# Performance work log

Measured on AMD Instinct MI355X. Metric: run time of the kernel, lower is better.

## Reference

```python
import jax, jax.numpy as jnp
import numpy as np

N_NODES = 100000
N_EDGES = 1600000
IN_RAW = 64
HID = 128


def setup_inputs() -> dict:
    key = jax.random.key(0)
    ks = jax.random.split(key, 16)
    inp = {
        "x": jax.random.normal(ks[0], (N_NODES, IN_RAW), dtype=jnp.float32),
        "edge_index": jax.random.randint(ks[1], (2, N_EDGES), 0, N_NODES, dtype=jnp.int64),
        "user_ids": jax.random.randint(ks[2], (N_NODES,), 0, 10000, dtype=jnp.int64),
        "locations": jax.random.randint(ks[3], (N_NODES,), 0, 1000, dtype=jnp.int64),
        "time_features": jax.random.normal(ks[4], (N_NODES, 4), dtype=jnp.float32),
        # embeddings / encoders
        "user_emb_table": jax.random.normal(ks[5], (10000, 32), dtype=jnp.float32) * 0.02,
        "loc_emb_table": jax.random.normal(ks[6], (1000, 16), dtype=jnp.float32) * 0.02,
        "W_time": jax.random.normal(ks[7], (4, 16), dtype=jnp.float32) * 0.1,
        "b_time": jnp.zeros((16,), dtype=jnp.float32),
        # SAGEConv 1: lin_l (aggregated, with bias), lin_r (root, no bias)
        "W1_l": jax.random.normal(ks[8], (HID, HID), dtype=jnp.float32) * (1.0 / np.sqrt(HID)),
        "b1": jnp.zeros((HID,), dtype=jnp.float32),
        "W1_r": jax.random.normal(ks[9], (HID, HID), dtype=jnp.float32) * (1.0 / np.sqrt(HID)),
        # SAGEConv 2
        "W2_l": jax.random.normal(ks[10], (HID, HID), dtype=jnp.float32) * (1.0 / np.sqrt(HID)),
        "b2": jnp.zeros((HID,), dtype=jnp.float32),
        "W2_r": jax.random.normal(ks[11], (HID, HID), dtype=jnp.float32) * (1.0 / np.sqrt(HID)),
        # classifier
        "Wc": jax.random.normal(ks[12], (HID, 1), dtype=jnp.float32) * (1.0 / np.sqrt(HID)),
        "bc": jnp.zeros((1,), dtype=jnp.float32),
    }
    return inp


def _sage_conv(h, src, dst, W_l, b_l, W_r, n_nodes):
    # mean aggregation of source features onto targets (PyG SAGEConv default)
    msg_sum = jax.ops.segment_sum(h[src], dst, num_segments=n_nodes)  # [N, D]
    deg = jax.ops.segment_sum(jnp.ones((src.shape[0],), h.dtype), dst, num_segments=n_nodes)
    agg = msg_sum / jnp.maximum(deg, 1.0)[:, None]
    return agg @ W_l + b_l + h @ W_r


def reference(x, edge_index, user_ids, locations, time_features,
              user_emb_table, loc_emb_table, W_time, b_time,
              W1_l, b1, W1_r, W2_l, b2, W2_r, Wc, bc):
    n = x.shape[0]
    src, dst = edge_index[0], edge_index[1]
    user_emb = user_emb_table[user_ids]            # [N, 32]
    loc_emb = loc_emb_table[locations]             # [N, 16]
    time_emb = time_features @ W_time + b_time     # [N, 16]
    h = jnp.concatenate([x, user_emb, loc_emb, time_emb], axis=-1)  # [N, 128]
    h = jax.nn.relu(_sage_conv(h, src, dst, W1_l, b1, W1_r, n))  # dropout = identity (eval)
    h = jax.nn.relu(_sage_conv(h, src, dst, W2_l, b2, W2_r, n))
    return jax.nn.sigmoid(h @ Wc + bc)  # [N, 1]
```

## Files before the change

kernel.cpp:

```cpp
#include <hip/hip_runtime.h>
#include <math.h>

#define N_NODES 100000
#define HID 128
#define NB 782
#define CAP 4096
#define NBLK 256
#define BTILE 6250
#define SUBCAP 32
#define SCAP 3072
#define WPB 64
#define EBLK 3125

typedef __attribute__((ext_vector_type(8))) short bf16x8;
typedef __attribute__((ext_vector_type(4))) float f32x4;
typedef __attribute__((ext_vector_type(2))) float f32x2;

__device__ __forceinline__ unsigned short f2bf(float f) {
  union { float f; unsigned u; } v; v.f = f;
  unsigned r = v.u + 0x7FFFu + ((v.u >> 16) & 1u);
  return (unsigned short)(r >> 16);
}
__device__ __forceinline__ unsigned packbf(float lo, float hi) {
  return (unsigned)f2bf(lo) | ((unsigned)f2bf(hi) << 16);
}
__device__ __forceinline__ unsigned pkfp8x4(float a, float b, float c, float d) {
  int v = __builtin_amdgcn_cvt_pk_fp8_f32(a, b, 0, false);
  v = __builtin_amdgcn_cvt_pk_fp8_f32(c, d, v, true);
  return (unsigned)v;
}
__device__ __forceinline__ float bflo(unsigned u) {
  union { unsigned u; float f; } v; v.u = u << 16; return v.f;
}
__device__ __forceinline__ float bfhi(unsigned u) {
  union { unsigned u; float f; } v; v.u = u & 0xFFFF0000u; return v.f;
}
__device__ __forceinline__ void acc_add_fp8(float* a, unsigned w) {
  f32x2 p0 = __builtin_amdgcn_cvt_pk_f32_fp8((int)w, false);
  f32x2 p1 = __builtin_amdgcn_cvt_pk_f32_fp8((int)w, true);
  a[0] += p0.x; a[1] += p0.y; a[2] += p1.x; a[3] += p1.y;
}
__device__ __forceinline__ void acc_add_row(float* a, uint4 u) {
  acc_add_fp8(a + 0, u.x);
  acc_add_fp8(a + 4, u.y);
  acc_add_fp8(a + 8, u.z);
  acc_add_fp8(a + 12, u.w);
}

__global__ __launch_bounds__(512) void k_bktembed(
    const int* __restrict__ src, const int* __restrict__ dst,
    int* __restrict__ gcnt, unsigned* __restrict__ bdata2, int E,
    const float* __restrict__ x, const int* __restrict__ uid,
    const int* __restrict__ lid, const float* __restrict__ timef,
    const float* __restrict__ utab, const float* __restrict__ ltab,
    const float* __restrict__ Wt, const float* __restrict__ bt,
    unsigned short* __restrict__ h0, unsigned char* __restrict__ h0f8) {
  __shared__ int hcnt[NB];
  int t = threadIdx.x;
  if (blockIdx.x < NBLK) {
    int blk = blockIdx.x;
    int e0 = blk * BTILE;
    int e1 = min(e0 + BTILE, E);
    for (int i = t; i < NB; i += 512) hcnt[i] = 0;
    __syncthreads();
#pragma unroll 4
    for (int e = e0 + t; e < e1; e += 512) {
      int d = dst[e], s = src[e];
      int b = d >> 7;
      int pos = atomicAdd(&hcnt[b], 1);
      if (pos < SUBCAP)
        bdata2[((size_t)blk * NB + b) * SUBCAP + pos] =
            ((unsigned)s << 7) | (unsigned)(d & 127);
    }
    __syncthreads();
    for (int i = t; i < NB; i += 512)
      gcnt[blk * NB + i] = hcnt[i];
    return;
  }
  int v = (blockIdx.x - NBLK) * 32 + (t >> 4);
  int g = t & 15;
  if (v >= N_NODES) return;
  float val[8];
  if (g < 8) {
    const float4* xp = (const float4*)&x[(size_t)v * 64 + g * 8];
    float4 a = xp[0], b = xp[1];
    val[0] = a.x; val[1] = a.y; val[2] = a.z; val[3] = a.w;
    val[4] = b.x; val[5] = b.y; val[6] = b.z; val[7] = b.w;
  } else if (g < 12) {
    const float4* up = (const float4*)&utab[(size_t)uid[v] * 32 + (g - 8) * 8];
    float4 a = up[0], b = up[1];
    val[0] = a.x; val[1] = a.y; val[2] = a.z; val[3] = a.w;
    val[4] = b.x; val[5] = b.y; val[6] = b.z; val[7] = b.w;
  } else if (g < 14) {
    const float4* lp = (const float4*)&ltab[(size_t)lid[v] * 16 + (g - 12) * 8];
    float4 a = lp[0], b = lp[1];
    val[0] = a.x; val[1] = a.y; val[2] = a.z; val[3] = a.w;
    val[4] = b.x; val[5] = b.y; val[6] = b.z; val[7] = b.w;
  } else {
    int c0 = (g - 14) * 8;
    float4 tf = *(const float4*)&timef[(size_t)v * 4];
#pragma unroll
    for (int i = 0; i < 8; ++i) {
      int c = c0 + i;
      val[i] = bt[c] + tf.x * Wt[c] + tf.y * Wt[16 + c] + tf.z * Wt[32 + c] +
               tf.w * Wt[48 + c];
    }
  }
  uint4 ob;
  ob.x = packbf(val[0], val[1]);
  ob.y = packbf(val[2], val[3]);
  ob.z = packbf(val[4], val[5]);
  ob.w = packbf(val[6], val[7]);
  *(uint4*)&h0[(size_t)v * 128 + g * 8] = ob;
  uint2 of;
  of.x = pkfp8x4(val[0], val[1], val[2], val[3]);
  of.y = pkfp8x4(val[4], val[5], val[6], val[7]);
  *(uint2*)&h0f8[(size_t)v * 128 + g * 8] = of;
}

__global__ __launch_bounds__(256) void k_bfill(
    const int* __restrict__ gcnt, const unsigned* __restrict__ bdata2,
    int* __restrict__ rstart, int* __restrict__ rdeg, int* __restrict__ col,
    const float* __restrict__ W1l, const float* __restrict__ W1r,
    const float* __restrict__ W2l, const float* __restrict__ W2r,
    unsigned short* __restrict__ WT) {
  int b = blockIdx.x;
  int t = threadIdx.x;
  if (b >= NB) {
    int lin = ((b - NB) * 256 + t) * 4;
    int m = lin >> 14;
    int rem = lin & 16383;
    int f = rem >> 7;
    int k0 = rem & 127;
    const float* W = (m == 0) ? W1l : (m == 1) ? W1r : (m == 2) ? W2l : W2r;
    unsigned short o[4];
#pragma unroll
    for (int j = 0; j < 4; ++j) o[j] = f2bf(W[(size_t)(k0 + j) * 128 + f]);
    uint2 pk;
    pk.x = (unsigned)o[0] | ((unsigned)o[1] << 16);
    pk.y = (unsigned)o[2] | ((unsigned)o[3] << 16);
    *(uint2*)&WT[m * 16384 + f * 128 + k0] = pk;
    return;
  }
  __shared__ unsigned sdata[SCAP];
  __shared__ int soff[NBLK];
  __shared__ int scnt[NBLK];
  __shared__ int wsum[4];
  __shared__ int lcnt[128];
  __shared__ int wtot;
  int lane = t & 63, wv = t >> 6;

  int c = (t < NBLK) ? min(gcnt[t * NB + b], SUBCAP) : 0;
  int x = c;
#pragma unroll
  for (int off = 1; off < 64; off <<= 1) {
    int v = __shfl_up(x, off);
    if (lane >= off) x += v;
  }
  if (lane == 63) wsum[wv] = x;
  __syncthreads();
  int add = 0;
#pragma unroll
  for (int k = 0; k < 4; ++k)
    if (k < wv) add += wsum[k];
  x += add;
  int tot = min(wsum[0] + wsum[1] + wsum[2] + wsum[3], SCAP);
  if (t < NBLK) { soff[t] = x - c; scnt[t] = c; }
  if (t < 128) lcnt[t] = 0;
  __syncthreads();

  for (int i = t; i < NBLK * 8; i += 256) {
    int j = i >> 3, p4 = (i & 7) * 4;
    int cj = scnt[j];
    if (p4 < cj) {
      uint4 v = *(const uint4*)&bdata2[((size_t)j * NB + b) * SUBCAP + p4];
      int bs = soff[j] + p4;
      int n = min(4, cj - p4);
      unsigned vv[4] = {v.x, v.y, v.z, v.w};
#pragma unroll
      for (int e = 0; e < 4; ++e)
        if (e < n && bs + e < SCAP) sdata[bs + e] = vv[e];
    }
  }
  __syncthreads();

  for (int i = t; i < tot; i += 256) atomicAdd(&lcnt[sdata[i] & 127u], 1);
  __syncthreads();

  int node0 = b * 128;
  int base = b * CAP;
  if (t < 128) {
    int cc = lcnt[t];
    int xx = cc;
#pragma unroll
    for (int off = 1; off < 64; off <<= 1) {
      int v = __shfl_up(xx, off);
      if (lane >= off) xx += v;
    }
    if (t == 63) wtot = xx;
    __syncthreads();
    if (t >= 64) xx += wtot;
    int excl = xx - cc;
    if (node0 + t < N_NODES) {
      rstart[node0 + t] = base + excl;
      rdeg[node0 + t] = cc;
    }
    lcnt[t] = excl;
  } else {
    __syncthreads();
  }
  __syncthreads();
  for (int i = t; i < tot; i += 256) {
    unsigned v = sdata[i];
    int pos = base + atomicAdd(&lcnt[v & 127u], 1);
    col[pos] = (int)(v >> 7);
  }
}

template <bool CLS>
__global__ __launch_bounds__(256, 4) void k_aggemm(
    const unsigned char* __restrict__ hf8, const int* __restrict__ rstart,
    const int* __restrict__ rdeg, const int* __restrict__ col,
    const unsigned short* __restrict__ hin,
    const unsigned short* __restrict__ WlT, const unsigned short* __restrict__ WrT,
    const float* __restrict__ bias, unsigned short* __restrict__ hout,
    unsigned char* __restrict__ houtf8,
    const float* __restrict__ Wc, const float* __restrict__ bc,
    float* __restrict__ out) {
  __shared__ unsigned short SB[2 * 64 * 136];
  unsigned short* As = SB;
  unsigned short* Hs = SB + 64 * 136;
  unsigned short* Ot = SB;
  float* zred = (float*)SB;
  int t = threadIdx.x;
  int lane = t & 63;
  int wave = t >> 6;
  int wn = wave * 32;
  int l15 = lane & 15;
  int quad = lane >> 4;
  int mbase = blockIdx.x * 64;

  int sr = t >> 2, sseg = t & 3;
  uint4 hv[4];
  {
    int gn = mbase + sr;
    if (gn < N_NODES) {
      const uint4* hp = (const uint4*)(hin + (size_t)gn * 128 + sseg * 32);
#pragma unroll
      for (int i = 0; i < 4; ++i) hv[i] = hp[i];
    } else {
#pragma unroll
      for (int i = 0; i < 4; ++i) hv[i] = make_uint4(0, 0, 0, 0);
    }
  }

  const uint4* h8 = (const uint4*)hf8;
#pragma unroll
  for (int half = 0; half < 2; ++half) {
    int r = half * 32 + (t >> 3);
    int q = t & 7;
    int v = mbase + r;
    float acc[16];
#pragma unroll
    for (int i = 0; i < 16; ++i) acc[i] = 0.f;
    float inv = 0.f;
    if (v < N_NODES) {
      int s0 = rstart[v];
      int deg = rdeg[v];
      int s1 = s0 + deg;
      int j = s0;
      for (; j + 4 <= s1; j += 4) {
        uint4 r0 = h8[(size_t)col[j] * 8 + q];
        uint4 r1 = h8[(size_t)col[j + 1] * 8 + q];
        uint4 r2 = h8[(size_t)col[j + 2] * 8 + q];
        uint4 r3 = h8[(size_t)col[j + 3] * 8 + q];
        acc_add_row(acc, r0);
        acc_add_row(acc, r1);
        acc_add_row(acc, r2);
        acc_add_row(acc, r3);
      }
      for (; j < s1; ++j) acc_add_row(acc, h8[(size_t)col[j] * 8 + q]);
      inv = 1.f / (float)(deg > 0 ? deg : 1);
    }
    uint4 o0, o1;
    o0.x = packbf(acc[0] * inv, acc[1] * inv);
    o0.y = packbf(acc[2] * inv, acc[3] * inv);
    o0.z = packbf(acc[4] * inv, acc[5] * inv);
    o0.w = packbf(acc[6] * inv, acc[7] * inv);
    o1.x = packbf(acc[8] * inv, acc[9] * inv);
    o1.y = packbf(acc[10] * inv, acc[11] * inv);
    o1.z = packbf(acc[12] * inv, acc[13] * inv);
    o1.w = packbf(acc[14] * inv, acc[15] * inv);
    *(uint4*)&As[r * 136 + q * 16] = o0;
    *(uint4*)&As[r * 136 + q * 16 + 8] = o1;
  }

#pragma unroll
  for (int i = 0; i < 4; ++i)
    *(uint4*)&Hs[sr * 136 + sseg * 32 + i * 8] = hv[i];
  __syncthreads();

  f32x4 acc4[4][2];
#pragma unroll
  for (int i = 0; i < 4; ++i)
#pragma unroll
    for (int j = 0; j < 2; ++j) acc4[i][j] = (f32x4){0.f, 0.f, 0.f, 0.f};

#pragma unroll
  for (int ks = 0; ks < 4; ++ks) {
    int kb = ks * 32 + quad * 8;
    bf16x8 bL[2], bR[2];
#pragma unroll
    for (int jn = 0; jn < 2; ++jn) {
      int f = wn + jn * 16 + l15;
      bL[jn] = *(const bf16x8*)&WlT[(size_t)f * 128 + kb];
      bR[jn] = *(const bf16x8*)&WrT[(size_t)f * 128 + kb];
    }
    bf16x8 aA[4], aH[4];
#pragma unroll
    for (int im = 0; im < 4; ++im) {
      aA[im] = *(const bf16x8*)&As[(im * 16 + l15) * 136 + kb];
      aH[im] = *(const bf16x8*)&Hs[(im * 16 + l15) * 136 + kb];
    }
#pragma unroll
    for (int im = 0; im < 4; ++im)
#pragma unroll
      for (int jn = 0; jn < 2; ++jn)
        acc4[im][jn] = __builtin_amdgcn_mfma_f32_16x16x32_bf16(
            aA[im], bL[jn], acc4[im][jn], 0, 0, 0);
#pragma unroll
    for (int im = 0; im < 4; ++im)
#pragma unroll
      for (int jn = 0; jn < 2; ++jn)
        acc4[im][jn] = __builtin_amdgcn_mfma_f32_16x16x32_bf16(
            aH[im], bR[jn], acc4[im][jn], 0, 0, 0);
  }

  float bv[2];
#pragma unroll
  for (int jn = 0; jn < 2; ++jn) bv[jn] = bias[wn + jn * 16 + l15];

  __syncthreads();

  if (!CLS) {
#pragma unroll
    for (int im = 0; im < 4; ++im)
#pragma unroll
      for (int rr = 0; rr < 4; ++rr) {
        int rloc = im * 16 + quad * 4 + rr;
#pragma unroll
        for (int jn = 0; jn < 2; ++jn)
          Ot[rloc * 136 + wn + jn * 16 + l15] =
              f2bf(fmaxf(acc4[im][jn][rr] + bv[jn], 0.f));
      }
    __syncthreads();
    int r = t >> 2, seg = t & 3;
    int node = mbase + r;
    if (node < N_NODES) {
      uint4 d0[4];
      const uint4* srcp = (const uint4*)&Ot[r * 136 + seg * 32];
      uint4* dstp = (uint4*)&hout[(size_t)node * 128 + seg * 32];
#pragma unroll
      for (int i = 0; i < 4; ++i) { d0[i] = srcp[i]; dstp[i] = d0[i]; }
      unsigned w[8];
#pragma unroll
      for (int i = 0; i < 4; ++i) {
        unsigned u[4] = {d0[i].x, d0[i].y, d0[i].z, d0[i].w};
#pragma unroll
        for (int p = 0; p < 2; ++p) {
          w[i * 2 + p] = pkfp8x4(bflo(u[p * 2]), bfhi(u[p * 2]),
                                 bflo(u[p * 2 + 1]), bfhi(u[p * 2 + 1]));
        }
      }
      uint4* fp = (uint4*)&houtf8[(size_t)node * 128 + seg * 32];
      fp[0] = make_uint4(w[0], w[1], w[2], w[3]);
      fp[1] = make_uint4(w[4], w[5], w[6], w[7]);
    }
  } else {
    float wcv[2];
#pragma unroll
    for (int jn = 0; jn < 2; ++jn) wcv[jn] = Wc[wn + jn * 16 + l15];
#pragma unroll
    for (int im = 0; im < 4; ++im) {
#pragma unroll
      for (int rr = 0; rr < 4; ++rr) {
        float p = 0.f;
#pragma unroll
        for (int jn = 0; jn < 2; ++jn)
          p += fmaxf(acc4[im][jn][rr] + bv[jn], 0.f) * wcv[jn];
        p += __shfl_xor(p, 1);
        p += __shfl_xor(p, 2);
        p += __shfl_xor(p, 4);
        p += __shfl_xor(p, 8);
        if (l15 == 0) zred[wave * 64 + im * 16 + quad * 4 + rr] = p;
      }
    }
    __syncthreads();
    if (t < 64) {
      int node = mbase + t;
      if (node < N_NODES) {
        float z = zred[t] + zred[64 + t] + zred[128 + t] + zred[192 + t] + bc[0];
        out[node] = 1.f / (1.f + expf(-z));
      }
    }
  }
}

extern "C" void kernel_launch(void* const* d_in, const int* in_sizes, int n_in,
                              void* d_out, int out_size, void* d_ws, size_t ws_size,
                              hipStream_t stream) {
  const float* x     = (const float*)d_in[0];
  const int*   eidx  = (const int*)d_in[1];
  const int*   uid   = (const int*)d_in[2];
  const int*   lid   = (const int*)d_in[3];
  const float* timef = (const float*)d_in[4];
  const float* utab  = (const float*)d_in[5];
  const float* ltab  = (const float*)d_in[6];
  const float* Wt    = (const float*)d_in[7];
  const float* bt    = (const float*)d_in[8];
  const float* W1l   = (const float*)d_in[9];
  const float* b1    = (const float*)d_in[10];
  const float* W1r   = (const float*)d_in[11];
  const float* W2l   = (const float*)d_in[12];
  const float* b2    = (const float*)d_in[13];
  const float* W2r   = (const float*)d_in[14];
  const float* Wc    = (const float*)d_in[15];
  const float* bc    = (const float*)d_in[16];
  float* out = (float*)d_out;

  const int E = in_sizes[1] / 2;
  const int* src = eidx;
  const int* dst = eidx + E;

  char* ws = (char*)d_ws;
  size_t off = 0;
  auto alloc = [&](size_t bytes) -> void* {
    void* p = ws + off;
    off += (bytes + 255) & ~(size_t)255;
    return p;
  };
  const size_t HBYTES = (size_t)N_NODES * 128 * sizeof(unsigned short);
  const size_t FBYTES = (size_t)N_NODES * 128;
  unsigned short* h0  = (unsigned short*)alloc(HBYTES);
  unsigned short* h1  = (unsigned short*)alloc(HBYTES);
  unsigned char* h0f8 = (unsigned char*)alloc(FBYTES);
  unsigned char* h1f8 = (unsigned char*)alloc(FBYTES);
  unsigned short* WT  = (unsigned short*)alloc(4 * 16384 * sizeof(unsigned short));
  unsigned* bdata2    = (unsigned*)alloc((size_t)NBLK * NB * SUBCAP * 4);
  int* gcnt           = (int*)alloc((size_t)NBLK * NB * 4);
  int* col            = (int*)alloc((size_t)NB * CAP * 4);
  int* rstart         = (int*)alloc((size_t)N_NODES * 4);
  int* rdeg           = (int*)alloc((size_t)N_NODES * 4);
  (void)ws_size; (void)n_in; (void)out_size;

  k_bktembed<<<NBLK + EBLK, 512, 0, stream>>>(src, dst, gcnt, bdata2, E,
                                              x, uid, lid, timef, utab, ltab,
                                              Wt, bt, h0, h0f8);
  k_bfill<<<NB + WPB, 256, 0, stream>>>(gcnt, bdata2, rstart, rdeg, col,
                                        W1l, W1r, W2l, W2r, WT);

  k_aggemm<false><<<(N_NODES + 63) / 64, 256, 0, stream>>>(
      h0f8, rstart, rdeg, col, h0, WT, WT + 16384, b1, h1, h1f8,
      nullptr, nullptr, nullptr);

  k_aggemm<true><<<(N_NODES + 63) / 64, 256, 0, stream>>>(
      h1f8, rstart, rdeg, col, h1, WT + 32768, WT + 49152, b2,
      nullptr, nullptr, Wc, bc, out);
}
```

Baseline: 268.3 us.

## Double aggregation threads per tile and split edge bucketing across more blocks

The fused aggregate+GEMM kernel now runs 512 threads per 64-node tile. Each thread gathers one row-segment instead of looping over two halves, and each wave computes a 16-column slice of the output, so more neighbor gathers are in flight at once. The edge-bucketing stage uses 1024 smaller edge tiles with a smaller per-bucket capacity, and the fill kernel's prefix scan handles four sub-counts per thread. The tighter launch bounds may restrict registers and cause spills, and the smaller per-bucket capacity raises the risk of overflow truncation.

```diff
diff --git a/kernel.cpp b/kernel.cpp
--- a/kernel.cpp
+++ b/kernel.cpp
@@ -5,9 +5,9 @@
 #define HID 128
 #define NB 782
 #define CAP 4096
-#define NBLK 256
-#define BTILE 6250
-#define SUBCAP 32
+#define NBLK 1024
+#define BTILE 1563
+#define SUBCAP 16
 #define SCAP 3072
 #define WPB 64
 #define EBLK 3125
@@ -150,8 +150,14 @@
   __shared__ int wtot;
   int lane = t & 63, wv = t >> 6;
 
-  int c = (t < NBLK) ? min(gcnt[t * NB + b], SUBCAP) : 0;
-  int x = c;
+  int c4[4];
+  int csum = 0;
+#pragma unroll
+  for (int k = 0; k < 4; ++k) {
+    c4[k] = min(gcnt[(size_t)(t * 4 + k) * NB + b], SUBCAP);
+    csum += c4[k];
+  }
+  int x = csum;
 #pragma unroll
   for (int off = 1; off < 64; off <<= 1) {
     int v = __shfl_up(x, off);
@@ -165,12 +171,18 @@
     if (k < wv) add += wsum[k];
   x += add;
   int tot = min(wsum[0] + wsum[1] + wsum[2] + wsum[3], SCAP);
-  if (t < NBLK) { soff[t] = x - c; scnt[t] = c; }
+  int run = x - csum;
+#pragma unroll
+  for (int k = 0; k < 4; ++k) {
+    soff[t * 4 + k] = run;
+    scnt[t * 4 + k] = c4[k];
+    run += c4[k];
+  }
   if (t < 128) lcnt[t] = 0;
   __syncthreads();
 
-  for (int i = t; i < NBLK * 8; i += 256) {
-    int j = i >> 3, p4 = (i & 7) * 4;
+  for (int i = t; i < NBLK * 4; i += 256) {
+    int j = i >> 2, p4 = (i & 3) * 4;
     int cj = scnt[j];
     if (p4 < cj) {
       uint4 v = *(const uint4*)&bdata2[((size_t)j * NB + b) * SUBCAP + p4];
@@ -218,7 +230,7 @@
 }
 
 template <bool CLS>
-__global__ __launch_bounds__(256, 4) void k_aggemm(
+__global__ __launch_bounds__(512, 8) void k_aggemm(
     const unsigned char* __restrict__ hf8, const int* __restrict__ rstart,
     const int* __restrict__ rdeg, const int* __restrict__ col,
     const unsigned short* __restrict__ hin,
@@ -235,30 +247,26 @@
   int t = threadIdx.x;
   int lane = t & 63;
   int wave = t >> 6;
-  int wn = wave * 32;
+  int wn = wave * 16;
   int l15 = lane & 15;
   int quad = lane >> 4;
   int mbase = blockIdx.x * 64;
 
-  int sr = t >> 2, sseg = t & 3;
-  uint4 hv[4];
+  int r = t >> 3, q = t & 7;
+
+  uint4 hv[2];
   {
-    int gn = mbase + sr;
+    int gn = mbase + r;
     if (gn < N_NODES) {
-      const uint4* hp = (const uint4*)(hin + (size_t)gn * 128 + sseg * 32);
-#pragma unroll
-      for (int i = 0; i < 4; ++i) hv[i] = hp[i];
+      const uint4* hp = (const uint4*)(hin + (size_t)gn * 128 + q * 16);
+      hv[0] = hp[0]; hv[1] = hp[1];
     } else {
-#pragma unroll
-      for (int i = 0; i < 4; ++i) hv[i] = make_uint4(0, 0, 0, 0);
-    }
-  }
-
-  const uint4* h8 = (const uint4*)hf8;
-#pragma unroll
-  for (int half = 0; half < 2; ++half) {
-    int r = half * 32 + (t >> 3);
-    int q = t & 7;
+      hv[0] = make_uint4(0, 0, 0, 0); hv[1] = make_uint4(0, 0, 0, 0);
+    }
+  }
+
+  {
+    const uint4* h8 = (const uint4*)hf8;
     int v = mbase + r;
     float acc[16];
 #pragma unroll
@@ -295,27 +303,20 @@
     *(uint4*)&As[r * 136 + q * 16 + 8] = o1;
   }
 
-#pragma unroll
-  for (int i = 0; i < 4; ++i)
-    *(uint4*)&Hs[sr * 136 + sseg * 32 + i * 8] = hv[i];
-  __syncthreads();
-
-  f32x4 acc4[4][2];
-#pragma unroll
-  for (int i = 0; i < 4; ++i)
-#pragma unroll
-    for (int j = 0; j < 2; ++j) acc4[i][j] = (f32x4){0.f, 0.f, 0.f, 0.f};
+  *(uint4*)&Hs[r * 136 + q * 16] = hv[0];
+  *(uint4*)&Hs[r * 136 + q * 16 + 8] = hv[1];
+  __syncthreads();
+
+  f32x4 acc4[4];
+#pragma unroll
+  for (int i = 0; i < 4; ++i) acc4[i] = (f32x4){0.f, 0.f, 0.f, 0.f};
 
 #pragma unroll
   for (int ks = 0; ks < 4; ++ks) {
     int kb = ks * 32 + quad * 8;
-    bf16x8 bL[2], bR[2];
-#pragma unroll
-    for (int jn = 0; jn < 2; ++jn) {
-      int f = wn + jn * 16 + l15;
-      bL[jn] = *(const bf16x8*)&WlT[(size_t)f * 128 + kb];
-      bR[jn] = *(const bf16x8*)&WrT[(size_t)f * 128 + kb];
-    }
+    int f = wn + l15;
+    bf16x8 bL = *(const bf16x8*)&WlT[(size_t)f * 128 + kb];
+    bf16x8 bR = *(const bf16x8*)&WrT[(size_t)f * 128 + kb];
     bf16x8 aA[4], aH[4];
 #pragma unroll
     for (int im = 0; im < 4; ++im) {
@@ -324,21 +325,13 @@
     }
 #pragma unroll
     for (int im = 0; im < 4; ++im)
-#pragma unroll
-      for (int jn = 0; jn < 2; ++jn)
-        acc4[im][jn] = __builtin_amdgcn_mfma_f32_16x16x32_bf16(
-            aA[im], bL[jn], acc4[im][jn], 0, 0, 0);
+      acc4[im] = __builtin_amdgcn_mfma_f32_16x16x32_bf16(aA[im], bL, acc4[im], 0, 0, 0);
 #pragma unroll
     for (int im = 0; im < 4; ++im)
-#pragma unroll
-      for (int jn = 0; jn < 2; ++jn)
-        acc4[im][jn] = __builtin_amdgcn_mfma_f32_16x16x32_bf16(
-            aH[im], bR[jn], acc4[im][jn], 0, 0, 0);
-  }
-
-  float bv[2];
-#pragma unroll
-  for (int jn = 0; jn < 2; ++jn) bv[jn] = bias[wn + jn * 16 + l15];
+      acc4[im] = __builtin_amdgcn_mfma_f32_16x16x32_bf16(aH[im], bR, acc4[im], 0, 0, 0);
+  }
+
+  float bv = bias[wn + l15];
 
   __syncthreads();
 
@@ -348,23 +341,19 @@
 #pragma unroll
       for (int rr = 0; rr < 4; ++rr) {
         int rloc = im * 16 + quad * 4 + rr;
-#pragma unroll
-        for (int jn = 0; jn < 2; ++jn)
-          Ot[rloc * 136 + wn + jn * 16 + l15] =
-              f2bf(fmaxf(acc4[im][jn][rr] + bv[jn], 0.f));
+        Ot[rloc * 136 + wn + l15] = f2bf(fmaxf(acc4[im][rr] + bv, 0.f));
       }
     __syncthreads();
-    int r = t >> 2, seg = t & 3;
     int node = mbase + r;
     if (node < N_NODES) {
-      uint4 d0[4];
-      const uint4* srcp = (const uint4*)&Ot[r * 136 + seg * 32];
-      uint4* dstp = (uint4*)&hout[(size_t)node * 128 + seg * 32];
-#pragma unroll
-      for (int i = 0; i < 4; ++i) { d0[i] = srcp[i]; dstp[i] = d0[i]; }
-      unsigned w[8];
-#pragma unroll
-      for (int i = 0; i < 4; ++i) {
+      uint4 d0[2];
+      const uint4* srcp = (const uint4*)&Ot[r * 136 + q * 16];
+      uint4* dstp = (uint4*)&hout[(size_t)node * 128 + q * 16];
+      d0[0] = srcp[0]; d0[1] = srcp[1];
+      dstp[0] = d0[0]; dstp[1] = d0[1];
+      unsigned w[4];
+#pragma unroll
+      for (int i = 0; i < 2; ++i) {
         unsigned u[4] = {d0[i].x, d0[i].y, d0[i].z, d0[i].w};
 #pragma unroll
         for (int p = 0; p < 2; ++p) {
@@ -372,22 +361,15 @@
                                  bflo(u[p * 2 + 1]), bfhi(u[p * 2 + 1]));
         }
       }
-      uint4* fp = (uint4*)&houtf8[(size_t)node * 128 + seg * 32];
-      fp[0] = make_uint4(w[0], w[1], w[2], w[3]);
-      fp[1] = make_uint4(w[4], w[5], w[6], w[7]);
+      *(uint4*)&houtf8[(size_t)node * 128 + q * 16] = make_uint4(w[0], w[1], w[2], w[3]);
     }
   } else {
-    float wcv[2];
-#pragma unroll
-    for (int jn = 0; jn < 2; ++jn) wcv[jn] = Wc[wn + jn * 16 + l15];
+    float wcv = Wc[wn + l15];
 #pragma unroll
     for (int im = 0; im < 4; ++im) {
 #pragma unroll
       for (int rr = 0; rr < 4; ++rr) {
-        float p = 0.f;
-#pragma unroll
-        for (int jn = 0; jn < 2; ++jn)
-          p += fmaxf(acc4[im][jn][rr] + bv[jn], 0.f) * wcv[jn];
+        float p = fmaxf(acc4[im][rr] + bv, 0.f) * wcv;
         p += __shfl_xor(p, 1);
         p += __shfl_xor(p, 2);
         p += __shfl_xor(p, 4);
@@ -399,7 +381,9 @@
     if (t < 64) {
       int node = mbase + t;
       if (node < N_NODES) {
-        float z = zred[t] + zred[64 + t] + zred[128 + t] + zred[192 + t] + bc[0];
+        float z = bc[0];
+#pragma unroll
+        for (int w8 = 0; w8 < 8; ++w8) z += zred[w8 * 64 + t];
         out[node] = 1.f / (1.f + expf(-z));
       }
     }
@@ -459,11 +443,11 @@
   k_bfill<<<NB + WPB, 256, 0, stream>>>(gcnt, bdata2, rstart, rdeg, col,
                                         W1l, W1r, W2l, W2r, WT);
 
-  k_aggemm<false><<<(N_NODES + 63) / 64, 256, 0, stream>>>(
+  k_aggemm<false><<<(N_NODES + 63) / 64, 512, 0, stream>>>(
       h0f8, rstart, rdeg, col, h0, WT, WT + 16384, b1, h1, h1f8,
       nullptr, nullptr, nullptr);
 
-  k_aggemm<true><<<(N_NODES + 63) / 64, 256, 0, stream>>>(
+  k_aggemm<true><<<(N_NODES + 63) / 64, 512, 0, stream>>>(
       h1f8, rstart, rdeg, col, h1, WT + 32768, WT + 49152, b2,
       nullptr, nullptr, Wc, bc, out);
 }
```

New measurement: 325.4 us. +21.3%, slower.

## Replace bucketed CSR build with global-atomic histogram, scan, and scatter

Applied to the files above, without the earlier changes.

Drops the two-level bucket sort (per-block sub-buckets with capped SUBCAP/SCAP staging, then a per-bucket fill) and builds the CSR with a global atomic degree histogram, a per-128-node block scan and an atomic-cursor scatter of source ids. The weight transpose moves into the fused embedding kernel, and a memset plus two small kernels are added. This removes the large bdata2/gcnt staging traffic and the per-bucket caps, but adds one launch and makes col order within a row nondeterministic, with global atomic contention on rdeg and cursor.

```diff
diff --git a/kernel.cpp b/kernel.cpp
--- a/kernel.cpp
+++ b/kernel.cpp
@@ -5,12 +5,11 @@
 #define HID 128
 #define NB 782
 #define CAP 4096
-#define NBLK 256
-#define BTILE 6250
-#define SUBCAP 32
-#define SCAP 3072
-#define WPB 64
+#define HB 256
+#define HTILE 6250
 #define EBLK 3125
+#define WPB 32
+#define SBLK 1024
 
 typedef __attribute__((ext_vector_type(8))) short bf16x8;
 typedef __attribute__((ext_vector_type(4))) float f32x4;
@@ -47,37 +46,41 @@
   acc_add_fp8(a + 12, u.w);
 }
 
-__global__ __launch_bounds__(512) void k_bktembed(
+__global__ __launch_bounds__(512) void k_histembed(
     const int* __restrict__ src, const int* __restrict__ dst,
-    int* __restrict__ gcnt, unsigned* __restrict__ bdata2, int E,
+    int* __restrict__ rdeg, int E,
     const float* __restrict__ x, const int* __restrict__ uid,
     const int* __restrict__ lid, const float* __restrict__ timef,
     const float* __restrict__ utab, const float* __restrict__ ltab,
     const float* __restrict__ Wt, const float* __restrict__ bt,
-    unsigned short* __restrict__ h0, unsigned char* __restrict__ h0f8) {
-  __shared__ int hcnt[NB];
+    unsigned short* __restrict__ h0, unsigned char* __restrict__ h0f8,
+    const float* __restrict__ W1l, const float* __restrict__ W1r,
+    const float* __restrict__ W2l, const float* __restrict__ W2r,
+    unsigned short* __restrict__ WT) {
   int t = threadIdx.x;
-  if (blockIdx.x < NBLK) {
-    int blk = blockIdx.x;
-    int e0 = blk * BTILE;
-    int e1 = min(e0 + BTILE, E);
-    for (int i = t; i < NB; i += 512) hcnt[i] = 0;
-    __syncthreads();
-#pragma unroll 4
-    for (int e = e0 + t; e < e1; e += 512) {
-      int d = dst[e], s = src[e];
-      int b = d >> 7;
-      int pos = atomicAdd(&hcnt[b], 1);
-      if (pos < SUBCAP)
-        bdata2[((size_t)blk * NB + b) * SUBCAP + pos] =
-            ((unsigned)s << 7) | (unsigned)(d & 127);
-    }
-    __syncthreads();
-    for (int i = t; i < NB; i += 512)
-      gcnt[blk * NB + i] = hcnt[i];
+  if (blockIdx.x < HB) {
+    int e0 = blockIdx.x * HTILE;
+    int e1 = min(e0 + HTILE, E);
+    for (int e = e0 + t; e < e1; e += 512) atomicAdd(&rdeg[dst[e]], 1);
     return;
   }
-  int v = (blockIdx.x - NBLK) * 32 + (t >> 4);
+  if (blockIdx.x >= HB + EBLK) {
+    int lin = ((blockIdx.x - HB - EBLK) * 512 + t) * 4;
+    int m = lin >> 14;
+    int rem = lin & 16383;
+    int f = rem >> 7;
+    int k0 = rem & 127;
+    const float* W = (m == 0) ? W1l : (m == 1) ? W1r : (m == 2) ? W2l : W2r;
+    unsigned short o[4];
+#pragma unroll
+    for (int j = 0; j < 4; ++j) o[j] = f2bf(W[(size_t)(k0 + j) * 128 + f]);
+    uint2 pk;
+    pk.x = (unsigned)o[0] | ((unsigned)o[1] << 16);
+    pk.y = (unsigned)o[2] | ((unsigned)o[3] << 16);
+    *(uint2*)&WT[m * 16384 + f * 128 + k0] = pk;
+    return;
+  }
+  int v = (blockIdx.x - HB) * 32 + (t >> 4);
   int g = t & 15;
   if (v >= N_NODES) return;
   float val[8];
@@ -118,102 +121,38 @@
   *(uint2*)&h0f8[(size_t)v * 128 + g * 8] = of;
 }
 
-__global__ __launch_bounds__(256) void k_bfill(
-    const int* __restrict__ gcnt, const unsigned* __restrict__ bdata2,
-    int* __restrict__ rstart, int* __restrict__ rdeg, int* __restrict__ col,
-    const float* __restrict__ W1l, const float* __restrict__ W1r,
-    const float* __restrict__ W2l, const float* __restrict__ W2r,
-    unsigned short* __restrict__ WT) {
-  int b = blockIdx.x;
-  int t = threadIdx.x;
-  if (b >= NB) {
-    int lin = ((b - NB) * 256 + t) * 4;
-    int m = lin >> 14;
-    int rem = lin & 16383;
-    int f = rem >> 7;
-    int k0 = rem & 127;
-    const float* W = (m == 0) ? W1l : (m == 1) ? W1r : (m == 2) ? W2l : W2r;
-    unsigned short o[4];
-#pragma unroll
-    for (int j = 0; j < 4; ++j) o[j] = f2bf(W[(size_t)(k0 + j) * 128 + f]);
-    uint2 pk;
-    pk.x = (unsigned)o[0] | ((unsigned)o[1] << 16);
-    pk.y = (unsigned)o[2] | ((unsigned)o[3] << 16);
-    *(uint2*)&WT[m * 16384 + f * 128 + k0] = pk;
-    return;
-  }
-  __shared__ unsigned sdata[SCAP];
-  __shared__ int soff[NBLK];
-  __shared__ int scnt[NBLK];
-  __shared__ int wsum[4];
-  __shared__ int lcnt[128];
-  __shared__ int wtot;
-  int lane = t & 63, wv = t >> 6;
-
-  int c = (t < NBLK) ? min(gcnt[t * NB + b], SUBCAP) : 0;
+__global__ __launch_bounds__(128) void k_bscan(
+    const int* __restrict__ rdeg, int* __restrict__ rstart,
+    int* __restrict__ cursor) {
+  __shared__ int w0tot;
+  int b = blockIdx.x, t = threadIdx.x;
+  int node = b * 128 + t;
+  int c = (node < N_NODES) ? rdeg[node] : 0;
   int x = c;
 #pragma unroll
   for (int off = 1; off < 64; off <<= 1) {
     int v = __shfl_up(x, off);
-    if (lane >= off) x += v;
-  }
-  if (lane == 63) wsum[wv] = x;
+    if ((t & 63) >= off) x += v;
+  }
+  if (t == 63) w0tot = x;
   __syncthreads();
-  int add = 0;
-#pragma unroll
-  for (int k = 0; k < 4; ++k)
-    if (k < wv) add += wsum[k];
-  x += add;
-  int tot = min(wsum[0] + wsum[1] + wsum[2] + wsum[3], SCAP);
-  if (t < NBLK) { soff[t] = x - c; scnt[t] = c; }
-  if (t < 128) lcnt[t] = 0;
-  __syncthreads();
-
-  for (int i = t; i < NBLK * 8; i += 256) {
-    int j = i >> 3, p4 = (i & 7) * 4;
-    int cj = scnt[j];
-    if (p4 < cj) {
-      uint4 v = *(const uint4*)&bdata2[((size_t)j * NB + b) * SUBCAP + p4];
-      int bs = soff[j] + p4;
-      int n = min(4, cj - p4);
-      unsigned vv[4] = {v.x, v.y, v.z, v.w};
-#pragma unroll
-      for (int e = 0; e < 4; ++e)
-        if (e < n && bs + e < SCAP) sdata[bs + e] = vv[e];
-    }
-  }
-  __syncthreads();
-
-  for (int i = t; i < tot; i += 256) atomicAdd(&lcnt[sdata[i] & 127u], 1);
-  __syncthreads();
-
-  int node0 = b * 128;
-  int base = b * CAP;
-  if (t < 128) {
-    int cc = lcnt[t];
-    int xx = cc;
-#pragma unroll
-    for (int off = 1; off < 64; off <<= 1) {
-      int v = __shfl_up(xx, off);
-      if (lane >= off) xx += v;
-    }
-    if (t == 63) wtot = xx;
-    __syncthreads();
-    if (t >= 64) xx += wtot;
-    int excl = xx - cc;
-    if (node0 + t < N_NODES) {
-      rstart[node0 + t] = base + excl;
-      rdeg[node0 + t] = cc;
-    }
-    lcnt[t] = excl;
-  } else {
-    __syncthreads();
-  }
-  __syncthreads();
-  for (int i = t; i < tot; i += 256) {
-    unsigned v = sdata[i];
-    int pos = base + atomicAdd(&lcnt[v & 127u], 1);
-    col[pos] = (int)(v >> 7);
+  if (t >= 64) x += w0tot;
+  int excl = x - c;
+  if (node < N_NODES) {
+    int rs = b * CAP + excl;
+    rstart[node] = rs;
+    cursor[node] = rs;
+  }
+}
+
+__global__ __launch_bounds__(256) void k_scatter(
+    const int* __restrict__ src, const int* __restrict__ dst,
+    int* __restrict__ cursor, int* __restrict__ col, int E) {
+  int stride = gridDim.x * 256;
+  for (int e = blockIdx.x * 256 + threadIdx.x; e < E; e += stride) {
+    int d = dst[e], s = src[e];
+    int pos = atomicAdd(&cursor[d], 1);
+    col[pos] = s;
   }
 }
 
@@ -446,18 +385,21 @@
   unsigned char* h0f8 = (unsigned char*)alloc(FBYTES);
   unsigned char* h1f8 = (unsigned char*)alloc(FBYTES);
   unsigned short* WT  = (unsigned short*)alloc(4 * 16384 * sizeof(unsigned short));
-  unsigned* bdata2    = (unsigned*)alloc((size_t)NBLK * NB * SUBCAP * 4);
-  int* gcnt           = (int*)alloc((size_t)NBLK * NB * 4);
   int* col            = (int*)alloc((size_t)NB * CAP * 4);
   int* rstart         = (int*)alloc((size_t)N_NODES * 4);
   int* rdeg           = (int*)alloc((size_t)N_NODES * 4);
+  int* cursor         = (int*)alloc((size_t)N_NODES * 4);
   (void)ws_size; (void)n_in; (void)out_size;
 
-  k_bktembed<<<NBLK + EBLK, 512, 0, stream>>>(src, dst, gcnt, bdata2, E,
-                                              x, uid, lid, timef, utab, ltab,
-                                              Wt, bt, h0, h0f8);
-  k_bfill<<<NB + WPB, 256, 0, stream>>>(gcnt, bdata2, rstart, rdeg, col,
-                                        W1l, W1r, W2l, W2r, WT);
+  hipMemsetAsync(rdeg, 0, (size_t)N_NODES * 4, stream);
+
+  k_histembed<<<HB + EBLK + WPB, 512, 0, stream>>>(
+      src, dst, rdeg, E, x, uid, lid, timef, utab, ltab, Wt, bt, h0, h0f8,
+      W1l, W1r, W2l, W2r, WT);
+
+  k_bscan<<<NB, 128, 0, stream>>>(rdeg, rstart, cursor);
+
+  k_scatter<<<SBLK, 256, 0, stream>>>(src, dst, cursor, col, E);
 
   k_aggemm<false><<<(N_NODES + 63) / 64, 256, 0, stream>>>(
       h0f8, rstart, rdeg, col, h0, WT, WT + 16384, b1, h1, h1f8,
```

Measured after the change: 435.1 us. 62.2% more time.
